# Kernel optimization log

Hardware: AMD Instinct MI355X
Metric: run time of the kernel (lower is better)

The kernel has to match this reference:

```python
import jax, jax.numpy as jnp
import numpy as np

N = 100000      # num_nodes
E = 640000      # num_edges
R = 64          # num_relations
D = 128         # emb_dim
L = 2           # num_layers


def setup_inputs() -> dict:
    key = jax.random.key(0)
    ks = jax.random.split(key, 24)
    s = 0.05
    inp = {}
    inp['edge_index'] = jax.random.randint(ks[0], (2, E), 0, N, dtype=jnp.int64)
    inp['edge_type'] = jax.random.randint(ks[1], (E,), 0, R, dtype=jnp.int64)
    inp['embed_w'] = jax.random.normal(ks[2], (N, D), jnp.float32) * s
    inp['rel_emb_w'] = jax.random.normal(ks[3], (L, R, D), jnp.float32) * s
    # rel_mlp: Linear(D,2D) ReLU Linear(2D,2D) ReLU Linear(2D,2D) ReLU Linear(2D,2D)   (hidden_layers=3)
    inp['rmw0'] = jax.random.normal(ks[4], (L, 2 * D, D), jnp.float32) * s
    inp['rmb0'] = jnp.zeros((L, 2 * D), jnp.float32)
    inp['rmw1'] = jax.random.normal(ks[5], (L, 2 * D, 2 * D), jnp.float32) * s
    inp['rmb1'] = jnp.zeros((L, 2 * D), jnp.float32)
    inp['rmw2'] = jax.random.normal(ks[6], (L, 2 * D, 2 * D), jnp.float32) * s
    inp['rmb2'] = jnp.zeros((L, 2 * D), jnp.float32)
    inp['rmw3'] = jax.random.normal(ks[7], (L, 2 * D, 2 * D), jnp.float32) * s
    inp['rmb3'] = jnp.zeros((L, 2 * D), jnp.float32)
    # per-edge linear W: Linear(D,D)
    inp['W_w'] = jax.random.normal(ks[8], (L, D, D), jnp.float32) * s
    inp['W_b'] = jnp.zeros((L, D), jnp.float32)
    # node update mlp: Linear(D,2D) ReLU Linear(2D,D)
    inp['mlp_w0'] = jax.random.normal(ks[9], (L, 2 * D, D), jnp.float32) * s
    inp['mlp_b0'] = jnp.zeros((L, 2 * D), jnp.float32)
    inp['mlp_w1'] = jax.random.normal(ks[10], (L, D, 2 * D), jnp.float32) * s
    inp['mlp_b1'] = jnp.zeros((L, D), jnp.float32)
    inp['eps'] = jnp.zeros((L,), jnp.float32)
    return inp


def reference(edge_index, edge_type, embed_w, rel_emb_w,
              rmw0, rmb0, rmw1, rmb1, rmw2, rmb2, rmw3, rmb3,
              W_w, W_b, mlp_w0, mlp_b0, mlp_w1, mlp_b1, eps):
    src = edge_index[0]  # x_j source nodes
    dst = edge_index[1]  # aggregation targets
    x = embed_w  # [N, D]
    for l in range(L):
        # relation FiLM params: compute once per relation id, gather per edge
        h = jax.nn.relu(rel_emb_w[l] @ rmw0[l].T + rmb0[l])
        h = jax.nn.relu(h @ rmw1[l].T + rmb1[l])
        h = jax.nn.relu(h @ rmw2[l].T + rmb2[l])
        gb = h @ rmw3[l].T + rmb3[l]          # [R, 2D]
        gamma, beta = gb[:, :D], gb[:, D:]
        # W x_j : transform all nodes (N < E), then gather per edge
        xw = x @ W_w[l].T + W_b[l]            # [N, D]
        m = gamma[edge_type] * xw[src] + beta[edge_type]  # [E, D]
        aggr = jax.ops.segment_sum(m, dst, num_segments=N)
        out = (1.0 + eps[l]) * x + aggr
        x = jax.nn.relu(out @ mlp_w0[l].T + mlp_b0[l]) @ mlp_w1[l].T + mlp_b1[l]
        # dropout is identity in eval mode
    return x
```

## Files before the change

kernel.cpp:

```cpp
#include <hip/hip_runtime.h>
#include <hip/hip_fp16.h>
#include <stdint.h>

#define N_NODES 100000
#define N_EDGES 640000
#define R_REL   64
#define D_DIM   128
#define L_LAYERS 2

#define CAP 32

#define LDA 136
#define LDT 264
#define LDFY 132
#define LDP 264
#define MROWS 128
#define GMLP ((N_NODES + MROWS - 1) / MROWS)

#define SCAT_BLKS  (N_EDGES / 256)
#define CONV_BLKS  256
#define XW_BLKS    (N_NODES / 32)

typedef __attribute__((ext_vector_type(8))) short    short8;
typedef __attribute__((ext_vector_type(8))) _Float16 half8;
typedef __attribute__((ext_vector_type(4))) unsigned short ushort4v;
typedef __attribute__((ext_vector_type(4))) float    f32x4;

__device__ __forceinline__ unsigned short f32_to_bf16(float f) {
  union { float f; uint32_t u; } v; v.f = f;
  uint32_t u = v.u;
  u += 0x7fffu + ((u >> 16) & 1u);
  return (unsigned short)(u >> 16);
}
__device__ __forceinline__ unsigned short f2h(float f) {
  __half h = __float2half(f);
  return __half_as_ushort(h);
}
__device__ __forceinline__ __half2 u2h(unsigned int u) {
  union { unsigned int u; __half2 h; } v; v.u = u; return v.h;
}
__device__ __forceinline__ short8 frag_from_f32(const float* p) {
  float4 a = *(const float4*)p;
  float4 b = *(const float4*)(p + 4);
  short8 r;
  r[0] = (short)f32_to_bf16(a.x); r[1] = (short)f32_to_bf16(a.y);
  r[2] = (short)f32_to_bf16(a.z); r[3] = (short)f32_to_bf16(a.w);
  r[4] = (short)f32_to_bf16(b.x); r[5] = (short)f32_to_bf16(b.y);
  r[6] = (short)f32_to_bf16(b.z); r[7] = (short)f32_to_bf16(b.w);
  return r;
}
__device__ __forceinline__ half8 hfrag_from_f32(const float* p) {
  float4 a = *(const float4*)p;
  float4 b = *(const float4*)(p + 4);
  half8 r;
  r[0] = (_Float16)a.x; r[1] = (_Float16)a.y;
  r[2] = (_Float16)a.z; r[3] = (_Float16)a.w;
  r[4] = (_Float16)b.x; r[5] = (_Float16)b.y;
  r[6] = (_Float16)b.z; r[7] = (_Float16)b.w;
  return r;
}

__global__ __launch_bounds__(256)
void scatter_bucket_kernel(const int* __restrict__ ei, const int* __restrict__ et,
                           int* __restrict__ cnt, unsigned int* __restrict__ bucket) {
  int idx = blockIdx.x * 256 + threadIdx.x;
  int dst = ei[N_EDGES + idx];
  int slot = atomicAdd(&cnt[dst], 1);
  if (slot < CAP)
    bucket[(size_t)dst * CAP + slot] =
        (unsigned int)ei[idx] | ((unsigned int)et[idx] << 17);
}

template<int K, bool RELU, bool FINAL>
__device__ __forceinline__ void prep_gemm(const unsigned short* __restrict__ inb,
                                          const float* __restrict__ W,
                                          const float* __restrict__ bias,
                                          unsigned short* __restrict__ outb,
                                          unsigned short* __restrict__ gbb_l,
                                          int wave, int lrow, int quad) {
  const int n0 = wave * 64;
  f32x4 acc[4][4] = {};
  for (int ks = 0; ks < K; ks += 32) {
    half8 bf[4];
    #pragma unroll
    for (int nt = 0; nt < 4; ++nt)
      bf[nt] = hfrag_from_f32(&W[(size_t)(n0 + nt * 16 + lrow) * K + ks + quad * 8]);
    #pragma unroll
    for (int mt = 0; mt < 4; ++mt) {
      half8 a = *(const half8*)&inb[(mt * 16 + lrow) * LDP + ks + quad * 8];
      #pragma unroll
      for (int nt = 0; nt < 4; ++nt)
        acc[mt][nt] = __builtin_amdgcn_mfma_f32_16x16x32_f16(a, bf[nt], acc[mt][nt], 0, 0, 0);
    }
  }
  #pragma unroll
  for (int mt = 0; mt < 4; ++mt)
    #pragma unroll
    for (int nt = 0; nt < 4; ++nt) {
      int col = n0 + nt * 16 + lrow;
      float bb = bias[col];
      #pragma unroll
      for (int rr = 0; rr < 4; ++rr) {
        int row = mt * 16 + quad * 4 + rr;
        float v = acc[mt][nt][rr] + bb;
        if (RELU) v = fmaxf(v, 0.f);
        if (!FINAL) {
          outb[row * LDP + col] = f2h(v);
        } else {
          int slot = (col < D_DIM) ? ((col >> 1) * 4 + (col & 1))
                                   : (((col - D_DIM) >> 1) * 4 + 2 + ((col - D_DIM) & 1));
          gbb_l[row * 256 + slot] = f2h(v);
        }
      }
    }
}

__global__ __launch_bounds__(256)
void prep_mfma_kernel(const float* __restrict__ rel_emb,
                      const float* __restrict__ rmw0, const float* __restrict__ rmb0,
                      const float* __restrict__ rmw1, const float* __restrict__ rmb1,
                      const float* __restrict__ rmw2, const float* __restrict__ rmb2,
                      const float* __restrict__ rmw3, const float* __restrict__ rmb3,
                      unsigned short* __restrict__ gbb) {
  __shared__ unsigned short bufX[64 * LDP];
  __shared__ unsigned short bufY[64 * LDP];
  const int l = blockIdx.x;
  const int tid = threadIdx.x;
  const int wave = tid >> 6, lane = tid & 63;
  const int lrow = lane & 15, quad = lane >> 4;

  for (int i = tid; i < 64 * 32; i += 256) {
    int row = i >> 5, c4 = i & 31;
    float4 v = *(const float4*)&rel_emb[(size_t)(l * R_REL + row) * D_DIM + c4 * 4];
    ushort4v s;
    s[0] = f2h(v.x); s[1] = f2h(v.y); s[2] = f2h(v.z); s[3] = f2h(v.w);
    *(ushort4v*)&bufX[row * LDP + c4 * 4] = s;
  }
  __syncthreads();

  prep_gemm<128, true, false>(bufX, rmw0 + (size_t)l * 256 * 128, rmb0 + l * 256,
                              bufY, nullptr, wave, lrow, quad);
  __syncthreads();
  prep_gemm<256, true, false>(bufY, rmw1 + (size_t)l * 256 * 256, rmb1 + l * 256,
                              bufX, nullptr, wave, lrow, quad);
  __syncthreads();
  prep_gemm<256, true, false>(bufX, rmw2 + (size_t)l * 256 * 256, rmb2 + l * 256,
                              bufY, nullptr, wave, lrow, quad);
  __syncthreads();
  prep_gemm<256, false, true>(bufY, rmw3 + (size_t)l * 256 * 256, rmb3 + l * 256,
                              nullptr, gbb + (size_t)l * R_REL * 256, wave, lrow, quad);
}

__global__ __launch_bounds__(256)
void conv_xw_kernel(const float* __restrict__ Ww, const float* __restrict__ mw0,
                    const float* __restrict__ mw1,
                    unsigned short* __restrict__ Wwb, unsigned short* __restrict__ mw0b,
                    unsigned short* __restrict__ mw1b,
                    const float* __restrict__ x, const float* __restrict__ Wb,
                    unsigned short* __restrict__ xwb) {
  __shared__ unsigned short a_lds[32 * LDA];
  const int b = blockIdx.x;
  const int tid = threadIdx.x;

  if (b < CONV_BLKS) {
    int i = b * 256 + tid;
    if (i < L_LAYERS * D_DIM * D_DIM)     Wwb[i]  = f32_to_bf16(Ww[i]);
    if (i < L_LAYERS * 2 * D_DIM * D_DIM) mw0b[i] = f32_to_bf16(mw0[i]);
    if (i < L_LAYERS * 2 * D_DIM * D_DIM) mw1b[i] = f32_to_bf16(mw1[i]);
    return;
  }

  const int m0 = (b - CONV_BLKS) * 32;

  for (int i = tid; i < 1024; i += 256) {
    int row = i >> 5, ch = i & 31;
    float4 v = *(const float4*)&x[(m0 + row) * D_DIM + ch * 4];
    ushort4v s;
    s[0] = f32_to_bf16(v.x); s[1] = f32_to_bf16(v.y);
    s[2] = f32_to_bf16(v.z); s[3] = f32_to_bf16(v.w);
    *(ushort4v*)&a_lds[row * LDA + ch * 4] = s;
  }
  __syncthreads();

  const int wave = tid >> 6, lane = tid & 63;
  const int lrow = lane & 15, quad = lane >> 4;
  const int n0 = wave * 32;

  f32x4 acc[2][2] = {};
  for (int ks = 0; ks < 128; ks += 32) {
    short8 a0 = *(const short8*)&a_lds[lrow * LDA + ks + quad * 8];
    short8 a1 = *(const short8*)&a_lds[(16 + lrow) * LDA + ks + quad * 8];
    short8 b0 = frag_from_f32(&Ww[(size_t)(n0 + lrow) * D_DIM + ks + quad * 8]);
    short8 b1 = frag_from_f32(&Ww[(size_t)(n0 + 16 + lrow) * D_DIM + ks + quad * 8]);
    acc[0][0] = __builtin_amdgcn_mfma_f32_16x16x32_bf16(a0, b0, acc[0][0], 0, 0, 0);
    acc[0][1] = __builtin_amdgcn_mfma_f32_16x16x32_bf16(a0, b1, acc[0][1], 0, 0, 0);
    acc[1][0] = __builtin_amdgcn_mfma_f32_16x16x32_bf16(a1, b0, acc[1][0], 0, 0, 0);
    acc[1][1] = __builtin_amdgcn_mfma_f32_16x16x32_bf16(a1, b1, acc[1][1], 0, 0, 0);
  }

  for (int mt = 0; mt < 2; ++mt)
    for (int nt = 0; nt < 2; ++nt)
      for (int rr = 0; rr < 4; ++rr) {
        int row = mt * 16 + quad * 4 + rr;
        int col = n0 + nt * 16 + lrow;
        xwb[(size_t)(m0 + row) * D_DIM + col] = f2h(acc[mt][nt][rr] + Wb[col]);
      }
}

__global__ __launch_bounds__(256)
void agg_kernel(const unsigned int* __restrict__ bucket, const int* __restrict__ cnt,
                const float* __restrict__ x, const unsigned short* __restrict__ xwb,
                const unsigned short* __restrict__ gbt, const float* __restrict__ eps,
                unsigned short* __restrict__ o) {
  const int lane = threadIdx.x & 63;
  const int n = __builtin_amdgcn_readfirstlane(blockIdx.x * 4 + (threadIdx.x >> 6));
  int cn = cnt[n]; if (cn > CAP) cn = CAP;
  const unsigned int* bk = bucket + (size_t)n * CAP;

  float acc0 = 0.0f, acc1 = 0.0f;
  int e = 0;
  for (; e + 4 <= cn; e += 4) {
    unsigned int d0 = bk[e], d1 = bk[e + 1], d2 = bk[e + 2], d3 = bk[e + 3];
    __half2 x0 = *(const __half2*)&xwb[(size_t)(d0 & 0x1FFFF) * D_DIM + lane * 2];
    __half2 x1 = *(const __half2*)&xwb[(size_t)(d1 & 0x1FFFF) * D_DIM + lane * 2];
    __half2 x2 = *(const __half2*)&xwb[(size_t)(d2 & 0x1FFFF) * D_DIM + lane * 2];
    __half2 x3 = *(const __half2*)&xwb[(size_t)(d3 & 0x1FFFF) * D_DIM + lane * 2];
    uint2 g0 = *(const uint2*)&gbt[(d0 >> 17) * 256 + lane * 4];
    uint2 g1 = *(const uint2*)&gbt[(d1 >> 17) * 256 + lane * 4];
    uint2 g2 = *(const uint2*)&gbt[(d2 >> 17) * 256 + lane * 4];
    uint2 g3 = *(const uint2*)&gbt[(d3 >> 17) * 256 + lane * 4];
    __half2 m0 = __hfma2(u2h(g0.x), x0, u2h(g0.y));
    __half2 m1 = __hfma2(u2h(g1.x), x1, u2h(g1.y));
    __half2 m2 = __hfma2(u2h(g2.x), x2, u2h(g2.y));
    __half2 m3 = __hfma2(u2h(g3.x), x3, u2h(g3.y));
    float2 f0 = __half22float2(m0), f1 = __half22float2(m1);
    float2 f2 = __half22float2(m2), f3 = __half22float2(m3);
    acc0 += (f0.x + f1.x) + (f2.x + f3.x);
    acc1 += (f0.y + f1.y) + (f2.y + f3.y);
  }
  if (e + 2 <= cn) {
    unsigned int d0 = bk[e], d1 = bk[e + 1];
    __half2 x0 = *(const __half2*)&xwb[(size_t)(d0 & 0x1FFFF) * D_DIM + lane * 2];
    __half2 x1 = *(const __half2*)&xwb[(size_t)(d1 & 0x1FFFF) * D_DIM + lane * 2];
    uint2 g0 = *(const uint2*)&gbt[(d0 >> 17) * 256 + lane * 4];
    uint2 g1 = *(const uint2*)&gbt[(d1 >> 17) * 256 + lane * 4];
    __half2 m0 = __hfma2(u2h(g0.x), x0, u2h(g0.y));
    __half2 m1 = __hfma2(u2h(g1.x), x1, u2h(g1.y));
    float2 f0 = __half22float2(m0), f1 = __half22float2(m1);
    acc0 += f0.x + f1.x;
    acc1 += f0.y + f1.y;
    e += 2;
  }
  if (e < cn) {
    unsigned int d0 = bk[e];
    __half2 x0 = *(const __half2*)&xwb[(size_t)(d0 & 0x1FFFF) * D_DIM + lane * 2];
    uint2 g0 = *(const uint2*)&gbt[(d0 >> 17) * 256 + lane * 4];
    __half2 m0 = __hfma2(u2h(g0.x), x0, u2h(g0.y));
    float2 f0 = __half22float2(m0);
    acc0 += f0.x;
    acc1 += f0.y;
  }

  const float e1v = 1.0f + eps[0];
  float2 xr = *(const float2*)&x[(size_t)n * D_DIM + lane * 2];
  unsigned int w = (unsigned int)f32_to_bf16(e1v * xr.x + acc0)
                 | ((unsigned int)f32_to_bf16(e1v * xr.y + acc1) << 16);
  *(unsigned int*)&o[(size_t)n * D_DIM + lane * 2] = w;
}

__global__ __launch_bounds__(512, 4)
void mlp_kernel(const unsigned short* __restrict__ o,
                const unsigned short* __restrict__ w0b, const float* __restrict__ b0,
                const unsigned short* __restrict__ w1b, const float* __restrict__ b1,
                float* __restrict__ y,
                const unsigned short* __restrict__ WwNb,
                const float* __restrict__ WbN,
                unsigned short* __restrict__ xwbN) {
  __shared__ unsigned short u_lds[MROWS * LDT];
  unsigned short* a_lds = u_lds;
  unsigned short* t_lds = u_lds;
  float*          yf    = (float*)u_lds;
  unsigned short* xs    = u_lds;

  const int tid = threadIdx.x;
  const int m0 = blockIdx.x * MROWS;

  for (int i = tid; i < MROWS * 16; i += 512) {
    int row = i >> 4, seg = i & 15;
    int rg = m0 + row; if (rg >= N_NODES) rg = N_NODES - 1;
    *(short8*)&a_lds[row * LDA + seg * 8] =
        *(const short8*)&o[(size_t)rg * D_DIM + seg * 8];
  }
  __syncthreads();

  const int wave = tid >> 6, lane = tid & 63;
  const int lrow = lane & 15, quad = lane >> 4;

  {
    const int n0 = wave * 32;
    f32x4 acc[8][2] = {};
    #pragma unroll
    for (int ks = 0; ks < 128; ks += 32) {
      short8 bf0 = *(const short8*)&w0b[(n0 + lrow) * D_DIM + ks + quad * 8];
      short8 bf1 = *(const short8*)&w0b[(n0 + 16 + lrow) * D_DIM + ks + quad * 8];
      #pragma unroll
      for (int mt = 0; mt < 8; ++mt) {
        short8 a = *(const short8*)&a_lds[(mt * 16 + lrow) * LDA + ks + quad * 8];
        acc[mt][0] = __builtin_amdgcn_mfma_f32_16x16x32_bf16(a, bf0, acc[mt][0], 0, 0, 0);
        acc[mt][1] = __builtin_amdgcn_mfma_f32_16x16x32_bf16(a, bf1, acc[mt][1], 0, 0, 0);
      }
    }
    __syncthreads();
    float bb0 = b0[n0 + lrow], bb1 = b0[n0 + 16 + lrow];
    #pragma unroll
    for (int mt = 0; mt < 8; ++mt)
      #pragma unroll
      for (int rr = 0; rr < 4; ++rr) {
        int row = mt * 16 + quad * 4 + rr;
        t_lds[row * LDT + n0 + lrow]      = f32_to_bf16(fmaxf(acc[mt][0][rr] + bb0, 0.0f));
        t_lds[row * LDT + n0 + 16 + lrow] = f32_to_bf16(fmaxf(acc[mt][1][rr] + bb1, 0.0f));
      }
  }
  __syncthreads();

  {
    const int n0 = wave * 16;
    f32x4 acc[8] = {};
    #pragma unroll
    for (int ks = 0; ks < 256; ks += 32) {
      short8 bf = *(const short8*)&w1b[(n0 + lrow) * 2 * D_DIM + ks + quad * 8];
      #pragma unroll
      for (int mt = 0; mt < 8; ++mt) {
        short8 a = *(const short8*)&t_lds[(mt * 16 + lrow) * LDT + ks + quad * 8];
        acc[mt] = __builtin_amdgcn_mfma_f32_16x16x32_bf16(a, bf, acc[mt], 0, 0, 0);
      }
    }
    __syncthreads();
    float bb = b1[n0 + lrow];
    #pragma unroll
    for (int mt = 0; mt < 8; ++mt)
      #pragma unroll
      for (int rr = 0; rr < 4; ++rr) {
        int row = mt * 16 + quad * 4 + rr;
        yf[row * LDFY + n0 + lrow] = acc[mt][rr] + bb;
      }
  }
  __syncthreads();

  for (int i = tid; i < MROWS * 32; i += 512) {
    int row = i >> 5, c4 = i & 31;
    int rg = m0 + row;
    if (rg < N_NODES)
      *(float4*)&y[(size_t)rg * D_DIM + c4 * 4] = *(const float4*)&yf[row * LDFY + c4 * 4];
  }

  if (xwbN) {
    const int n0 = wave * 16;
    f32x4 acc[8] = {};
    #pragma unroll
    for (int ks = 0; ks < 128; ks += 32) {
      short8 bf = *(const short8*)&WwNb[(n0 + lrow) * D_DIM + ks + quad * 8];
      #pragma unroll
      for (int mt = 0; mt < 8; ++mt) {
        short8 a = frag_from_f32(&yf[(mt * 16 + lrow) * LDFY + ks + quad * 8]);
        acc[mt] = __builtin_amdgcn_mfma_f32_16x16x32_bf16(a, bf, acc[mt], 0, 0, 0);
      }
    }
    __syncthreads();
    float bb = WbN[n0 + lrow];
    #pragma unroll
    for (int mt = 0; mt < 8; ++mt)
      #pragma unroll
      for (int rr = 0; rr < 4; ++rr) {
        int row = mt * 16 + quad * 4 + rr;
        xs[row * LDA + n0 + lrow] = f2h(acc[mt][rr] + bb);
      }
    __syncthreads();
    for (int i = tid; i < MROWS * 16; i += 512) {
      int row = i >> 4, seg = i & 15;
      int rg = m0 + row;
      if (rg < N_NODES)
        *(short8*)&xwbN[(size_t)rg * D_DIM + seg * 8] = *(const short8*)&xs[row * LDA + seg * 8];
    }
  }
}

extern "C" void kernel_launch(void* const* d_in, const int* in_sizes, int n_in,
                              void* d_out, int out_size, void* d_ws, size_t ws_size,
                              hipStream_t stream) {
  const int*   ei      = (const int*)d_in[0];
  const int*   et      = (const int*)d_in[1];
  const float* embed   = (const float*)d_in[2];
  const float* rel_emb = (const float*)d_in[3];
  const float* rmw0 = (const float*)d_in[4];  const float* rmb0 = (const float*)d_in[5];
  const float* rmw1 = (const float*)d_in[6];  const float* rmb1 = (const float*)d_in[7];
  const float* rmw2 = (const float*)d_in[8];  const float* rmb2 = (const float*)d_in[9];
  const float* rmw3 = (const float*)d_in[10]; const float* rmb3 = (const float*)d_in[11];
  const float* Ww   = (const float*)d_in[12]; const float* Wb   = (const float*)d_in[13];
  const float* mw0  = (const float*)d_in[14]; const float* mb0  = (const float*)d_in[15];
  const float* mw1  = (const float*)d_in[16]; const float* mb1  = (const float*)d_in[17];
  const float* eps  = (const float*)d_in[18];
  float* out = (float*)d_out;

  float*          W1   = (float*)d_ws;
  unsigned short* xwb  = (unsigned short*)(W1 + (size_t)N_NODES * D_DIM);
  unsigned short* gbb  = xwb + (size_t)N_NODES * D_DIM;
  unsigned short* Wwb  = gbb + L_LAYERS * R_REL * 256;
  unsigned short* mw0b = Wwb + L_LAYERS * D_DIM * D_DIM;
  unsigned short* mw1b = mw0b + L_LAYERS * 2 * D_DIM * D_DIM;
  int*   cnt     = (int*)(mw1b + L_LAYERS * 2 * D_DIM * D_DIM);
  unsigned int* bucket = (unsigned int*)(cnt + N_NODES);
  unsigned short* obuf = (unsigned short*)(bucket + (size_t)N_NODES * CAP);

  hipMemsetAsync(cnt, 0, N_NODES * sizeof(int), stream);
  scatter_bucket_kernel<<<SCAT_BLKS, 256, 0, stream>>>(ei, et, cnt, bucket);
  prep_mfma_kernel<<<L_LAYERS, 256, 0, stream>>>(
      rel_emb, rmw0, rmb0, rmw1, rmb1, rmw2, rmb2, rmw3, rmb3, gbb);
  conv_xw_kernel<<<CONV_BLKS + XW_BLKS, 256, 0, stream>>>(
      Ww, mw0, mw1, Wwb, mw0b, mw1b, embed, Wb, xwb);

  const int gA = N_NODES / 4;

  agg_kernel<<<gA, 256, 0, stream>>>(bucket, cnt, embed, xwb, gbb, eps, obuf);
  mlp_kernel<<<GMLP, 512, 0, stream>>>(obuf, mw0b, mb0, mw1b, mb1, W1,
                                       Wwb + D_DIM * D_DIM, Wb + D_DIM, xwb);

  agg_kernel<<<gA, 256, 0, stream>>>(bucket, cnt, W1, xwb,
                                     gbb + R_REL * 256, eps + 1, obuf);
  mlp_kernel<<<GMLP, 512, 0, stream>>>(obuf, mw0b + 2 * D_DIM * D_DIM, mb0 + 2 * D_DIM,
                                       mw1b + 2 * D_DIM * D_DIM, mb1 + D_DIM, out,
                                       nullptr, nullptr, nullptr);
}
```

Before: 411.9 us.

## Merge relation-MLP prep into conv/xw kernel and widen xw tiles to 128 rows

Folds the two-block relation FiLM MLP into the same launch as weight conversion and the first-layer x@W transform, using 512-thread blocks. This removes one kernel launch and lets the serial prep blocks run alongside the other work. The xw GEMM now handles 128-row tiles with each wave owning 16 output columns and reusing one B fragment across 8 M tiles. Results are staged through LDS so global stores are 16-byte vectors. Prep GEMM per-wave N width is halved to match 8 waves, and the larger shared-memory footprint may reduce occupancy.

Result: faster. 365.1 us (-11.4%).

```diff
diff --git a/kernel.cpp b/kernel.cpp
--- a/kernel.cpp
+++ b/kernel.cpp
@@ -18,8 +18,9 @@
 #define GMLP ((N_NODES + MROWS - 1) / MROWS)
 
 #define SCAT_BLKS  (N_EDGES / 256)
-#define CONV_BLKS  256
-#define XW_BLKS    (N_NODES / 32)
+#define PREP_BLKS  2
+#define CONV_BLKS  128
+#define PCX_BLKS   (PREP_BLKS + CONV_BLKS + GMLP)
 
 typedef __attribute__((ext_vector_type(8))) short    short8;
 typedef __attribute__((ext_vector_type(8))) _Float16 half8;
@@ -78,25 +79,25 @@
                                           unsigned short* __restrict__ outb,
                                           unsigned short* __restrict__ gbb_l,
                                           int wave, int lrow, int quad) {
-  const int n0 = wave * 64;
-  f32x4 acc[4][4] = {};
+  const int n0 = wave * 32;
+  f32x4 acc[4][2] = {};
   for (int ks = 0; ks < K; ks += 32) {
-    half8 bf[4];
-    #pragma unroll
-    for (int nt = 0; nt < 4; ++nt)
+    half8 bf[2];
+    #pragma unroll
+    for (int nt = 0; nt < 2; ++nt)
       bf[nt] = hfrag_from_f32(&W[(size_t)(n0 + nt * 16 + lrow) * K + ks + quad * 8]);
     #pragma unroll
     for (int mt = 0; mt < 4; ++mt) {
       half8 a = *(const half8*)&inb[(mt * 16 + lrow) * LDP + ks + quad * 8];
       #pragma unroll
-      for (int nt = 0; nt < 4; ++nt)
+      for (int nt = 0; nt < 2; ++nt)
         acc[mt][nt] = __builtin_amdgcn_mfma_f32_16x16x32_f16(a, bf[nt], acc[mt][nt], 0, 0, 0);
     }
   }
   #pragma unroll
   for (int mt = 0; mt < 4; ++mt)
     #pragma unroll
-    for (int nt = 0; nt < 4; ++nt) {
+    for (int nt = 0; nt < 2; ++nt) {
       int col = n0 + nt * 16 + lrow;
       float bb = bias[col];
       #pragma unroll
@@ -115,96 +116,100 @@
     }
 }
 
-__global__ __launch_bounds__(256)
-void prep_mfma_kernel(const float* __restrict__ rel_emb,
-                      const float* __restrict__ rmw0, const float* __restrict__ rmb0,
-                      const float* __restrict__ rmw1, const float* __restrict__ rmb1,
-                      const float* __restrict__ rmw2, const float* __restrict__ rmb2,
-                      const float* __restrict__ rmw3, const float* __restrict__ rmb3,
-                      unsigned short* __restrict__ gbb) {
-  __shared__ unsigned short bufX[64 * LDP];
-  __shared__ unsigned short bufY[64 * LDP];
-  const int l = blockIdx.x;
+__global__ __launch_bounds__(512, 4)
+void prep_conv_xw_kernel(const float* __restrict__ rel_emb,
+                         const float* __restrict__ rmw0, const float* __restrict__ rmb0,
+                         const float* __restrict__ rmw1, const float* __restrict__ rmb1,
+                         const float* __restrict__ rmw2, const float* __restrict__ rmb2,
+                         const float* __restrict__ rmw3, const float* __restrict__ rmb3,
+                         unsigned short* __restrict__ gbb,
+                         const float* __restrict__ Ww, const float* __restrict__ mw0,
+                         const float* __restrict__ mw1,
+                         unsigned short* __restrict__ Wwb, unsigned short* __restrict__ mw0b,
+                         unsigned short* __restrict__ mw1b,
+                         const float* __restrict__ x, const float* __restrict__ Wb,
+                         unsigned short* __restrict__ xwb) {
+  __shared__ unsigned short u_lds[2 * 64 * LDP];
+  const int b = blockIdx.x;
   const int tid = threadIdx.x;
   const int wave = tid >> 6, lane = tid & 63;
   const int lrow = lane & 15, quad = lane >> 4;
 
-  for (int i = tid; i < 64 * 32; i += 256) {
-    int row = i >> 5, c4 = i & 31;
-    float4 v = *(const float4*)&rel_emb[(size_t)(l * R_REL + row) * D_DIM + c4 * 4];
-    ushort4v s;
-    s[0] = f2h(v.x); s[1] = f2h(v.y); s[2] = f2h(v.z); s[3] = f2h(v.w);
-    *(ushort4v*)&bufX[row * LDP + c4 * 4] = s;
-  }
-  __syncthreads();
-
-  prep_gemm<128, true, false>(bufX, rmw0 + (size_t)l * 256 * 128, rmb0 + l * 256,
-                              bufY, nullptr, wave, lrow, quad);
-  __syncthreads();
-  prep_gemm<256, true, false>(bufY, rmw1 + (size_t)l * 256 * 256, rmb1 + l * 256,
-                              bufX, nullptr, wave, lrow, quad);
-  __syncthreads();
-  prep_gemm<256, true, false>(bufX, rmw2 + (size_t)l * 256 * 256, rmb2 + l * 256,
-                              bufY, nullptr, wave, lrow, quad);
-  __syncthreads();
-  prep_gemm<256, false, true>(bufY, rmw3 + (size_t)l * 256 * 256, rmb3 + l * 256,
-                              nullptr, gbb + (size_t)l * R_REL * 256, wave, lrow, quad);
-}
-
-__global__ __launch_bounds__(256)
-void conv_xw_kernel(const float* __restrict__ Ww, const float* __restrict__ mw0,
-                    const float* __restrict__ mw1,
-                    unsigned short* __restrict__ Wwb, unsigned short* __restrict__ mw0b,
-                    unsigned short* __restrict__ mw1b,
-                    const float* __restrict__ x, const float* __restrict__ Wb,
-                    unsigned short* __restrict__ xwb) {
-  __shared__ unsigned short a_lds[32 * LDA];
-  const int b = blockIdx.x;
-  const int tid = threadIdx.x;
-
-  if (b < CONV_BLKS) {
-    int i = b * 256 + tid;
+  if (b < PREP_BLKS) {
+    unsigned short* bufX = u_lds;
+    unsigned short* bufY = u_lds + 64 * LDP;
+    const int l = b;
+    for (int i = tid; i < 64 * 32; i += 512) {
+      int row = i >> 5, c4 = i & 31;
+      float4 v = *(const float4*)&rel_emb[(size_t)(l * R_REL + row) * D_DIM + c4 * 4];
+      ushort4v s;
+      s[0] = f2h(v.x); s[1] = f2h(v.y); s[2] = f2h(v.z); s[3] = f2h(v.w);
+      *(ushort4v*)&bufX[row * LDP + c4 * 4] = s;
+    }
+    __syncthreads();
+    prep_gemm<128, true, false>(bufX, rmw0 + (size_t)l * 256 * 128, rmb0 + l * 256,
+                                bufY, nullptr, wave, lrow, quad);
+    __syncthreads();
+    prep_gemm<256, true, false>(bufY, rmw1 + (size_t)l * 256 * 256, rmb1 + l * 256,
+                                bufX, nullptr, wave, lrow, quad);
+    __syncthreads();
+    prep_gemm<256, true, false>(bufX, rmw2 + (size_t)l * 256 * 256, rmb2 + l * 256,
+                                bufY, nullptr, wave, lrow, quad);
+    __syncthreads();
+    prep_gemm<256, false, true>(bufY, rmw3 + (size_t)l * 256 * 256, rmb3 + l * 256,
+                                nullptr, gbb + (size_t)l * R_REL * 256, wave, lrow, quad);
+    return;
+  }
+
+  if (b < PREP_BLKS + CONV_BLKS) {
+    int i = (b - PREP_BLKS) * 512 + tid;
     if (i < L_LAYERS * D_DIM * D_DIM)     Wwb[i]  = f32_to_bf16(Ww[i]);
     if (i < L_LAYERS * 2 * D_DIM * D_DIM) mw0b[i] = f32_to_bf16(mw0[i]);
     if (i < L_LAYERS * 2 * D_DIM * D_DIM) mw1b[i] = f32_to_bf16(mw1[i]);
     return;
   }
 
-  const int m0 = (b - CONV_BLKS) * 32;
-
-  for (int i = tid; i < 1024; i += 256) {
-    int row = i >> 5, ch = i & 31;
-    float4 v = *(const float4*)&x[(m0 + row) * D_DIM + ch * 4];
+  unsigned short* a_lds = u_lds;
+  const int m0 = (b - PREP_BLKS - CONV_BLKS) * MROWS;
+
+  for (int i = tid; i < MROWS * 32; i += 512) {
+    int row = i >> 5, c4 = i & 31;
+    int rg = m0 + row; if (rg >= N_NODES) rg = N_NODES - 1;
+    float4 v = *(const float4*)&x[(size_t)rg * D_DIM + c4 * 4];
     ushort4v s;
     s[0] = f32_to_bf16(v.x); s[1] = f32_to_bf16(v.y);
     s[2] = f32_to_bf16(v.z); s[3] = f32_to_bf16(v.w);
-    *(ushort4v*)&a_lds[row * LDA + ch * 4] = s;
-  }
-  __syncthreads();
-
-  const int wave = tid >> 6, lane = tid & 63;
-  const int lrow = lane & 15, quad = lane >> 4;
-  const int n0 = wave * 32;
-
-  f32x4 acc[2][2] = {};
+    *(ushort4v*)&a_lds[row * LDA + c4 * 4] = s;
+  }
+  __syncthreads();
+
+  const int n0 = wave * 16;
+  f32x4 acc[8] = {};
+  #pragma unroll
   for (int ks = 0; ks < 128; ks += 32) {
-    short8 a0 = *(const short8*)&a_lds[lrow * LDA + ks + quad * 8];
-    short8 a1 = *(const short8*)&a_lds[(16 + lrow) * LDA + ks + quad * 8];
-    short8 b0 = frag_from_f32(&Ww[(size_t)(n0 + lrow) * D_DIM + ks + quad * 8]);
-    short8 b1 = frag_from_f32(&Ww[(size_t)(n0 + 16 + lrow) * D_DIM + ks + quad * 8]);
-    acc[0][0] = __builtin_amdgcn_mfma_f32_16x16x32_bf16(a0, b0, acc[0][0], 0, 0, 0);
-    acc[0][1] = __builtin_amdgcn_mfma_f32_16x16x32_bf16(a0, b1, acc[0][1], 0, 0, 0);
-    acc[1][0] = __builtin_amdgcn_mfma_f32_16x16x32_bf16(a1, b0, acc[1][0], 0, 0, 0);
-    acc[1][1] = __builtin_amdgcn_mfma_f32_16x16x32_bf16(a1, b1, acc[1][1], 0, 0, 0);
-  }
-
-  for (int mt = 0; mt < 2; ++mt)
-    for (int nt = 0; nt < 2; ++nt)
-      for (int rr = 0; rr < 4; ++rr) {
-        int row = mt * 16 + quad * 4 + rr;
-        int col = n0 + nt * 16 + lrow;
-        xwb[(size_t)(m0 + row) * D_DIM + col] = f2h(acc[mt][nt][rr] + Wb[col]);
-      }
+    short8 bf = frag_from_f32(&Ww[(size_t)(n0 + lrow) * D_DIM + ks + quad * 8]);
+    #pragma unroll
+    for (int mt = 0; mt < 8; ++mt) {
+      short8 a = *(const short8*)&a_lds[(mt * 16 + lrow) * LDA + ks + quad * 8];
+      acc[mt] = __builtin_amdgcn_mfma_f32_16x16x32_bf16(a, bf, acc[mt], 0, 0, 0);
+    }
+  }
+  __syncthreads();
+  float bb = Wb[n0 + lrow];
+  #pragma unroll
+  for (int mt = 0; mt < 8; ++mt)
+    #pragma unroll
+    for (int rr = 0; rr < 4; ++rr) {
+      int row = mt * 16 + quad * 4 + rr;
+      a_lds[row * LDA + n0 + lrow] = f2h(acc[mt][rr] + bb);
+    }
+  __syncthreads();
+  for (int i = tid; i < MROWS * 16; i += 512) {
+    int row = i >> 4, seg = i & 15;
+    int rg = m0 + row;
+    if (rg < N_NODES)
+      *(short8*)&xwb[(size_t)rg * D_DIM + seg * 8] = *(const short8*)&a_lds[row * LDA + seg * 8];
+  }
 }
 
 __global__ __launch_bounds__(256)
@@ -414,9 +419,8 @@
 
   hipMemsetAsync(cnt, 0, N_NODES * sizeof(int), stream);
   scatter_bucket_kernel<<<SCAT_BLKS, 256, 0, stream>>>(ei, et, cnt, bucket);
-  prep_mfma_kernel<<<L_LAYERS, 256, 0, stream>>>(
-      rel_emb, rmw0, rmb0, rmw1, rmb1, rmw2, rmb2, rmw3, rmb3, gbb);
-  conv_xw_kernel<<<CONV_BLKS + XW_BLKS, 256, 0, stream>>>(
+  prep_conv_xw_kernel<<<PCX_BLKS, 512, 0, stream>>>(
+      rel_emb, rmw0, rmb0, rmw1, rmb1, rmw2, rmb2, rmw3, rmb3, gbb,
       Ww, mw0, mw1, Wwb, mw0b, mw1b, embed, Wb, xwb);
 
   const int gA = N_NODES / 4;
```
